# Performance work log

Measured on AMD Instinct MI355X. Metric: run time of the kernel, lower is better.

Reference implementation:

```python
import jax, jax.numpy as jnp
import numpy as np

B, C, T, H, W, L = 4, 256, 8, 16, 16, 8
NO = 8                # num_offsets
D = C // NO           # per-head feature dim for offset/weight MLPs
EPS = 1e-5


def setup_inputs() -> dict:
    key = jax.random.key(0)
    ks = jax.random.split(key, 6)
    return {
        "features": jax.random.normal(ks[0], (B, C, T, H, W, L), jnp.float32),
        "pos": jax.random.normal(ks[1], (B, C, T, H, W, L), jnp.float32),
        "Wp": jax.random.normal(ks[2], (C, 3 * C), jnp.float32) * 0.02,  # 1x1x1 conv: 3C -> C
        "bp": jnp.zeros((C,), jnp.float32),
        "Wo": jax.random.normal(ks[3], (D, 3), jnp.float32) * 0.02,      # offset_embed Linear(d,3)
        "bo": jnp.zeros((3,), jnp.float32),
        "Ww": jax.random.normal(ks[4], (D, 2), jnp.float32) * 0.02,      # weight_embed Linear(d,2)
        "bw": jnp.zeros((2,), jnp.float32),
    }


def _trilinear_sample(feat, coords):
    """feat: (N,C,D1,D2,D3); coords: (N,G,3) in [-1,1] (axis order D1,D2,D3).
    align_corners=False, zeros padding (matches F.grid_sample semantics)."""
    N, Cc, D1, D2, D3 = feat.shape
    sizes = jnp.asarray([D1, D2, D3], feat.dtype)
    pix = ((coords + 1.0) * sizes - 1.0) * 0.5       # unnormalize to pixel coords
    lo = jnp.floor(pix)
    frac = pix - lo                                   # (N,G,3)
    lo = lo.astype(jnp.int32)
    dims = jnp.asarray([D1, D2, D3], jnp.int32)
    feat_flat = feat.reshape(N, Cc, D1 * D2 * D3)
    out = jnp.zeros((N, Cc, coords.shape[1]), feat.dtype)
    for dz in (0, 1):
        for dy in (0, 1):
            for dx in (0, 1):
                off = jnp.asarray([dz, dy, dx], jnp.int32)
                idx = lo + off                        # (N,G,3)
                wz = jnp.where(dz, frac[..., 0], 1.0 - frac[..., 0])
                wy = jnp.where(dy, frac[..., 1], 1.0 - frac[..., 1])
                wx = jnp.where(dx, frac[..., 2], 1.0 - frac[..., 2])
                wgt = wz * wy * wx                    # (N,G)
                valid = jnp.all((idx >= 0) & (idx < dims), axis=-1)
                idc = jnp.clip(idx, 0, dims - 1)
                lin = (idc[..., 0] * D2 + idc[..., 1]) * D3 + idc[..., 2]  # (N,G)
                vals = jnp.take_along_axis(feat_flat, lin[:, None, :], axis=2)  # (N,C,G)
                out = out + vals * (wgt * valid)[:, None, :]
    return out


def reference(features, pos, Wp, bp, Wo, bo, Ww, bw):
    Bv, Cv, Tv, Hv, Wv, Lv = features.shape
    BT = Bv * Tv
    feat = features.transpose(0, 2, 1, 3, 4, 5).reshape(BT, Cv, Hv, Wv, Lv)
    posr = pos.transpose(0, 2, 1, 3, 4, 5).reshape(BT, Cv, Hv, Wv, Lv)
    # global context + projection (1x1x1 conv over 3C channels) + ReLU
    glob = feat.mean(axis=(2, 3, 4), keepdims=True)
    src = jnp.concatenate([feat, posr, jnp.broadcast_to(glob, feat.shape)], axis=1)  # (BT,3C,H,W,L)
    proj = jax.nn.relu(jnp.einsum('nixyz,oi->noxyz', src, Wp) + bp[None, :, None, None, None])
    osrc = proj.transpose(0, 2, 3, 4, 1).reshape(BT, Hv, Wv, Lv, NO, D)
    # per-voxel per-head offsets in (0,1) and scalar weights
    offset = jax.nn.sigmoid(osrc @ Wo + bo)                      # (BT,H,W,L,NO,3)
    wgt = jax.nn.softmax(osrc @ Ww + bw, axis=-1)[..., 1]        # (BT,H,W,L,NO)
    # base flow field in [-1,1], deform in logit space, re-sigmoid
    base = jnp.stack(jnp.meshgrid(jnp.linspace(-1.0, 1.0, Hv),
                                  jnp.linspace(-1.0, 1.0, Wv),
                                  jnp.linspace(-1.0, 1.0, Lv), indexing='ij'), axis=-1)
    base01 = jnp.clip((base + 1.0) * 0.5, EPS, 1.0 - EPS)
    logit = jnp.log(base01 / (1.0 - base01))                     # (H,W,L,3)
    sp = jax.nn.sigmoid(logit[None, :, :, :, None, :] + offset)  # (BT,H,W,L,NO,3)
    grid = (sp * 2.0 - 1.0).transpose(0, 4, 1, 2, 3, 5).reshape(BT, NO * Hv * Wv * Lv, 3)
    sampled = _trilinear_sample(feat, grid).reshape(BT, Cv, NO, Hv, Wv, Lv)
    out = feat + jnp.einsum('bcnhwl,bhwln->bchwl', sampled, wgt)
    return out.reshape(Bv, Tv, Cv, Hv, Wv, Lv).transpose(0, 2, 1, 3, 4, 5)
```

## Files before the change

### kernel.cpp

```cpp
#include <hip/hip_runtime.h>

#define BB 4
#define CC 256
#define TT 8
#define HH 16
#define WW 16
#define LL 8
#define NO 8
#define DD 32
#define BT 32
#define VV 2048
#define KIN 512
#define EPS_ 1e-5f

typedef short bf16x8 __attribute__((ext_vector_type(8)));
typedef float f32x4 __attribute__((ext_vector_type(4)));

static __device__ __forceinline__ float b2f(unsigned short u) {
    return __uint_as_float(((unsigned int)u) << 16);
}
static __device__ __forceinline__ float b2f_lo(unsigned int x) {
    return __uint_as_float(x << 16);
}
static __device__ __forceinline__ float b2f_hi(unsigned int x) {
    return __uint_as_float(x & 0xffff0000u);
}
static __device__ __forceinline__ unsigned short f2b(float f) {
    unsigned int x = __float_as_uint(f);
    unsigned int r = x + 0x7fffu + ((x >> 16) & 1u);
    return (unsigned short)(r >> 16);
}
static __device__ __forceinline__ unsigned int f2b_pk(float lo, float hi) {
    return (unsigned int)f2b(lo) | ((unsigned int)f2b(hi) << 16);
}
static __device__ __forceinline__ float sigm(float x) {
    return 1.0f / (1.0f + __expf(-x));
}
static __device__ __forceinline__ void glds16(const void* g, void* l) {
    __builtin_amdgcn_global_load_lds(
        (const __attribute__((address_space(1))) void*)g,
        (__attribute__((address_space(3))) void*)l, 16, 0, 0);
}

__global__ __launch_bounds__(256) void k0_prep(const float* __restrict__ Wp,
                                               unsigned short* __restrict__ Wa) {
    int i = blockIdx.x * 256 + threadIdx.x;
    int o = i >> 9, k = i & 511;
    Wa[i] = f2b(Wp[o * 768 + k]);
}

__global__ __launch_bounds__(256) void k1_transpose(const float* __restrict__ features,
                                                    const float* __restrict__ pos,
                                                    unsigned short* __restrict__ srcT,
                                                    float* __restrict__ gpart) {
    const int vt  = blockIdx.x;
    const int ch  = blockIdx.y & 1;
    const int arr = blockIdx.y >> 1;
    const int n   = blockIdx.z;
    const int v0 = vt * 64;
    const int b = n >> 3, t = n & 7;
    const int tid = threadIdx.x;
    const int w = tid >> 6;
    const int lane = tid & 63;
    const int cs  = lane >> 4;
    const int v16 = lane & 15;

    __shared__ float s1[64 * 132];

    const float* src = arr ? pos : features;
    const float* bp0 = src + ((size_t)(b * CC + ch * 128 + w * 32 + cs) * TT + t) * (size_t)VV
                           + v0 + v16 * 4;

    float4 fv[8];
    #pragma unroll
    for (int i = 0; i < 8; ++i)
        fv[i] = *(const float4*)(bp0 + (size_t)i * 4 * TT * VV);

    float part[8];
    #pragma unroll
    for (int i = 0; i < 8; ++i) {
        const int c_l = w * 32 + i * 4 + cs;
        float* dst = &s1[(v16 * 4) * 132 + c_l];
        dst[0 * 132] = fv[i].x;
        dst[1 * 132] = fv[i].y;
        dst[2 * 132] = fv[i].z;
        dst[3 * 132] = fv[i].w;
        part[i] = fv[i].x + fv[i].y + fv[i].z + fv[i].w;
    }

    if (arr == 0) {
        #pragma unroll
        for (int i = 0; i < 8; ++i) {
            #pragma unroll
            for (int m = 1; m < 16; m <<= 1)
                part[i] += __shfl_xor(part[i], m);
        }
        if (v16 == 0) {
            #pragma unroll
            for (int i = 0; i < 8; ++i)
                gpart[((size_t)n * 32 + vt) * CC + ch * 128 + w * 32 + i * 4 + cs] = part[i];
        }
    }
    __syncthreads();

    const int vo = tid >> 2, q = tid & 3;
    const float* row = &s1[vo * 132];
    unsigned short* ob = srcT + ((size_t)n * VV + v0 + vo) * KIN + arr * 256 + ch * 128;
    #pragma unroll
    for (int j = 0; j < 4; ++j) {
        const int c0 = j * 32 + q * 8;
        float4 f0 = *(const float4*)(row + c0);
        float4 f1 = *(const float4*)(row + c0 + 4);
        uint4 o;
        o.x = f2b_pk(f0.x, f0.y);
        o.y = f2b_pk(f0.z, f0.w);
        o.z = f2b_pk(f1.x, f1.y);
        o.w = f2b_pk(f1.z, f1.w);
        *(uint4*)(ob + c0) = o;
    }
}

__global__ __launch_bounds__(256) void k2_gterm(const float* __restrict__ gpart,
                                                const float* __restrict__ Wp,
                                                const float* __restrict__ bp,
                                                float* __restrict__ gterm) {
    const int n = blockIdx.x;
    const int o = threadIdx.x;
    __shared__ float gl[CC];
    float s = 0.0f;
    const float* gp = gpart + (size_t)n * 32 * CC + o;
    #pragma unroll 8
    for (int vt = 0; vt < 32; ++vt) s += gp[vt * CC];
    gl[o] = s * (1.0f / (float)VV);
    __syncthreads();
    const float4* wrow = (const float4*)(Wp + (size_t)o * 768 + 512);
    const float4* g4 = (const float4*)gl;
    float acc = bp[o];
    #pragma unroll 8
    for (int c = 0; c < 64; ++c) {
        float4 w = wrow[c], g = g4[c];
        acc += w.x * g.x + w.y * g.y + w.z * g.z + w.w * g.w;
    }
    gterm[n * CC + o] = acc;
}

__global__ __launch_bounds__(256) void k3_gemm(const unsigned short* __restrict__ Wa,
                                               const unsigned short* __restrict__ srcT,
                                               const float* __restrict__ gterm,
                                               unsigned short* __restrict__ projT) {
    const int n  = blockIdx.x;
    const int mb = blockIdx.y;
    const int nb = blockIdx.z;
    const int tid = threadIdx.x;
    const int m0 = mb * 128, v0 = nb * 128;

    __shared__ short As[128 * 32];
    __shared__ short Bs[128 * 32];

    const int w = tid >> 6;
    const int lane = tid & 63;
    const int wm = w >> 1, wn = w & 1;
    const int lr = lane & 15, lq = lane >> 4;

    f32x4 acc[4][4];
    #pragma unroll
    for (int i = 0; i < 4; ++i)
        #pragma unroll
        for (int j = 0; j < 4; ++j)
            acc[i][j] = (f32x4){0.f, 0.f, 0.f, 0.f};

    const int rsub = lane >> 2;
    const int ksub = (lane & 3) * 8;
    const unsigned short* agp = Wa   + (size_t)(m0 + w * 16 + rsub) * KIN + ksub;
    const unsigned short* bgp = srcT + ((size_t)n * VV + v0 + w * 16 + rsub) * KIN + ksub;
    short* alds0 = &As[(w * 16) * 32];
    short* alds1 = &As[(64 + w * 16) * 32];
    short* blds0 = &Bs[(w * 16) * 32];
    short* blds1 = &Bs[(64 + w * 16) * 32];

    for (int k0 = 0; k0 < KIN; k0 += 32) {
        __syncthreads();
        glds16(agp + k0,                   alds0);
        glds16(agp + k0 + (size_t)64 * KIN, alds1);
        glds16(bgp + k0,                   blds0);
        glds16(bgp + k0 + (size_t)64 * KIN, blds1);
        __syncthreads();

        bf16x8 af[4], bf[4];
        #pragma unroll
        for (int i = 0; i < 4; ++i)
            af[i] = *(const bf16x8*)&As[(wm * 64 + i * 16 + lr) * 32 + lq * 8];
        #pragma unroll
        for (int j = 0; j < 4; ++j)
            bf[j] = *(const bf16x8*)&Bs[(wn * 64 + j * 16 + lr) * 32 + lq * 8];
        #pragma unroll
        for (int i = 0; i < 4; ++i)
            #pragma unroll
            for (int j = 0; j < 4; ++j)
                acc[i][j] = __builtin_amdgcn_mfma_f32_16x16x32_bf16(af[i], bf[j], acc[i][j], 0, 0, 0);
    }

    #pragma unroll
    for (int i = 0; i < 4; ++i) {
        const int og = m0 + wm * 64 + i * 16 + lq * 4;
        float4 g = *(const float4*)(gterm + n * CC + og);
        #pragma unroll
        for (int j = 0; j < 4; ++j) {
            const int vg = v0 + wn * 64 + j * 16 + lr;
            float x0 = fmaxf(acc[i][j][0] + g.x, 0.0f);
            float x1 = fmaxf(acc[i][j][1] + g.y, 0.0f);
            float x2 = fmaxf(acc[i][j][2] + g.z, 0.0f);
            float x3 = fmaxf(acc[i][j][3] + g.w, 0.0f);
            ushort4 st;
            st.x = f2b(x0); st.y = f2b(x1); st.z = f2b(x2); st.w = f2b(x3);
            *(ushort4*)&projT[((size_t)n * VV + vg) * CC + og] = st;
        }
    }
}

__global__ __launch_bounds__(256) void k4_coef(const unsigned short* __restrict__ projT,
                                               const float* __restrict__ Wo,
                                               const float* __restrict__ bo,
                                               const float* __restrict__ Ww,
                                               const float* __restrict__ bw,
                                               int2* __restrict__ pairs) {
    __shared__ float sWo[96], sWw[64], sb[5];
    const int tid = threadIdx.x;
    if (tid < 96) sWo[tid] = Wo[tid];
    if (tid < 64) sWw[tid] = Ww[tid];
    if (tid < 3)  sb[tid] = bo[tid];
    if (tid < 2)  sb[3 + tid] = bw[tid];
    __syncthreads();

    const int g = blockIdx.x * 256 + tid;
    const int n = g >> 14;
    const int rem = g & 16383;
    const int v = rem >> 3;
    const int hd = rem & 7;

    const uint4* up = (const uint4*)(projT + ((size_t)n * VV + v) * CC + hd * DD);
    float osrc[32];
    #pragma unroll
    for (int q = 0; q < 4; ++q) {
        uint4 u = up[q];
        unsigned int ws4[4] = {u.x, u.y, u.z, u.w};
        #pragma unroll
        for (int e = 0; e < 4; ++e) {
            osrc[q * 8 + e * 2]     = b2f_lo(ws4[e]);
            osrc[q * 8 + e * 2 + 1] = b2f_hi(ws4[e]);
        }
    }

    float o0 = sb[0], o1 = sb[1], o2 = sb[2];
    float zw = sb[4] - sb[3];
    #pragma unroll
    for (int d = 0; d < DD; ++d) {
        float t = osrc[d];
        o0 += t * sWo[3 * d + 0];
        o1 += t * sWo[3 * d + 1];
        o2 += t * sWo[3 * d + 2];
        zw += t * (sWw[2 * d + 1] - sWw[2 * d]);
    }
    const float wgt = sigm(zw);

    const int h = v >> 7, w = (v >> 3) & 15, l = v & 7;
    float ph = fminf(fmaxf(h * (1.0f / 15.0f), EPS_), 1.0f - EPS_);
    float pw = fminf(fmaxf(w * (1.0f / 15.0f), EPS_), 1.0f - EPS_);
    float pl = fminf(fmaxf(l * (1.0f / 7.0f),  EPS_), 1.0f - EPS_);
    float lh = __logf(ph / (1.0f - ph));
    float lw = __logf(pw / (1.0f - pw));
    float ll = __logf(pl / (1.0f - pl));

    float sph = sigm(lh + sigm(o0));
    float spw = sigm(lw + sigm(o1));
    float spl = sigm(ll + sigm(o2));
    float pixh = sph * 16.0f - 0.5f;
    float pixw = spw * 16.0f - 0.5f;
    float pixl = spl * 8.0f  - 0.5f;

    float flh = floorf(pixh), flw = floorf(pixw), fll = floorf(pixl);
    float fh = pixh - flh, fw = pixw - flw, fl = pixl - fll;
    int ih = (int)flh, iw = (int)flw, il = (int)fll;

    int2* pp = pairs + (size_t)g * 8;
    #pragma unroll
    for (int dz = 0; dz < 2; ++dz)
        #pragma unroll
        for (int dy = 0; dy < 2; ++dy)
            #pragma unroll
            for (int dx = 0; dx < 2; ++dx) {
                int iz = ih + dz, iy = iw + dy, ix = il + dx;
                float wt = (dz ? fh : 1.0f - fh) * (dy ? fw : 1.0f - fw) * (dx ? fl : 1.0f - fl) * wgt;
                bool valid = ((unsigned)iz < 16u) && ((unsigned)iy < 16u) && ((unsigned)ix < 8u);
                int lin = valid ? (((iz * 16 + iy) * 8 + ix) << 10) : 0;
                float wv2 = valid ? wt : 0.0f;
                pp[dz * 4 + dy * 2 + dx] = make_int2(lin, __float_as_int(wv2));
            }
}

__global__ __launch_bounds__(256) void k5_gather(const unsigned short* __restrict__ srcT,
                                                 const int2* __restrict__ pairs,
                                                 unsigned short* __restrict__ res) {
    __shared__ int   sK[4 * 64];
    __shared__ float sW[4 * 64];
    const int tid = threadIdx.x;
    const int wid = tid >> 6;
    const int lane = tid & 63;
    const int gv = blockIdx.x * 4 + wid;
    const int n = gv >> 11;
    const int v = gv & 2047;

    int2 q = pairs[(size_t)gv * 64 + lane];
    int key = q.x;
    float w = __int_as_float(q.y);

    #pragma unroll
    for (int k = 2; k <= 64; k <<= 1) {
        #pragma unroll
        for (int j = k >> 1; j > 0; j >>= 1) {
            int pk = __shfl_xor(key, j);
            float pw = __shfl_xor(w, j);
            bool keepMin = (((lane & k) == 0) == ((lane & j) == 0));
            bool take = keepMin ? (pk < key) : (pk > key);
            if (take) { key = pk; w = pw; }
        }
    }
    #pragma unroll
    for (int d = 1; d < 64; d <<= 1) {
        float tw = __shfl_up(w, d);
        int   tk = __shfl_up(key, d);
        if (lane >= d && tk == key) w += tw;
    }
    int nk = __shfl_down(key, 1);
    bool tail = (lane == 63) || (nk != key);
    unsigned long long mask = __ballot(tail);
    int cnt = __popcll(mask);
    int cidx = __popcll(mask & ((1ull << lane) - 1ull));

    sK[wid * 64 + lane] = 0;
    sW[wid * 64 + lane] = 0.0f;
    __syncthreads();
    if (tail) { sK[wid * 64 + cidx] = key; sW[wid * 64 + cidx] = w; }
    __syncthreads();
    int ck = sK[wid * 64 + lane];
    float cw = sW[wid * 64 + lane];

    const char* slabB = (const char*)srcT + (size_t)n * VV * KIN * 2 + lane * 8;
    float a0 = 0.f, a1 = 0.f, a2 = 0.f, a3 = 0.f;
    const int iters = (cnt + 7) & ~7;
    #pragma unroll 1
    for (int e = 0; e < iters; e += 8) {
        uint2 f[8]; float wv[8];
        #pragma unroll
        for (int u = 0; u < 8; ++u) {
            int rk = __shfl(ck, e + u);
            wv[u] = __shfl(cw, e + u);
            f[u] = *(const uint2*)(slabB + (unsigned)rk);
        }
        #pragma unroll
        for (int u = 0; u < 8; ++u) {
            a0 = fmaf(wv[u], b2f_lo(f[u].x), a0);
            a1 = fmaf(wv[u], b2f_hi(f[u].x), a1);
            a2 = fmaf(wv[u], b2f_lo(f[u].y), a2);
            a3 = fmaf(wv[u], b2f_hi(f[u].y), a3);
        }
    }

    uint2 st;
    st.x = f2b_pk(a0, a1);
    st.y = f2b_pk(a2, a3);
    *(uint2*)&res[((size_t)n * VV + v) * CC + lane * 4] = st;
}

__global__ __launch_bounds__(256) void k6_final(const float* __restrict__ features,
                                                const unsigned short* __restrict__ res,
                                                float* __restrict__ out) {
    const int n = blockIdx.x;
    const int c0 = blockIdx.y * 64;
    const int v0 = blockIdx.z * 64;
    const int b = n >> 3, t = n & 7;
    const int tid = threadIdx.x;
    const int ty = tid >> 6, tx = tid & 63;

    __shared__ unsigned short t6[64 * 66];

    for (int vv = ty; vv < 64; vv += 4)
        t6[vv * 66 + tx] = res[((size_t)n * VV + v0 + vv) * CC + c0 + tx];
    __syncthreads();
    for (int cc = ty; cc < 64; cc += 4) {
        int c = c0 + cc;
        size_t oidx = (((size_t)b * CC + c) * TT + t) * VV + v0 + tx;
        out[oidx] = features[oidx] + b2f(t6[tx * 66 + cc]);
    }
}

extern "C" void kernel_launch(void* const* d_in, const int* in_sizes, int n_in,
                              void* d_out, int out_size, void* d_ws, size_t ws_size,
                              hipStream_t stream) {
    (void)in_sizes; (void)n_in; (void)out_size; (void)ws_size;
    const float* features = (const float*)d_in[0];
    const float* pos      = (const float*)d_in[1];
    const float* Wp       = (const float*)d_in[2];
    const float* bp       = (const float*)d_in[3];
    const float* Wo       = (const float*)d_in[4];
    const float* bo       = (const float*)d_in[5];
    const float* Ww       = (const float*)d_in[6];
    const float* bw       = (const float*)d_in[7];
    float* out = (float*)d_out;

    char* ws = (char*)d_ws;
    unsigned short* srcT  = (unsigned short*)ws;
    unsigned short* Wa    = (unsigned short*)(ws + 67108864);
    float*          gterm = (float*)(ws + 67403776);
    unsigned short* projT = (unsigned short*)(ws + 67436544);
    int2*           pairs = (int2*)(ws + 100990976);
    float*          gpart = (float*)(ws + 100990976);
    unsigned short* res   = projT;

    k0_prep<<<512, 256, 0, stream>>>(Wp, Wa);
    k1_transpose<<<dim3(32, 4, 32), 256, 0, stream>>>(features, pos, srcT, gpart);
    k2_gterm<<<32, 256, 0, stream>>>(gpart, Wp, bp, gterm);
    k3_gemm<<<dim3(32, 2, 16), 256, 0, stream>>>(Wa, srcT, gterm, projT);
    k4_coef<<<2048, 256, 0, stream>>>(projT, Wo, bo, Ww, bw, pairs);
    k5_gather<<<16384, 256, 0, stream>>>(srcT, pairs, res);
    k6_final<<<dim3(32, 4, 32), 256, 0, stream>>>(features, res, out);
}
```

Baseline: 330.5 us.

## Convert to bf16 before LDS transpose and use DPP/readlane in sort-gather kernel

The transpose kernel now packs fp32 values to bf16 pairs before staging them in shared memory. This halves LDS traffic and size, and it changes the lane mapping and the reduction pattern for the global-mean partial sums. The gather kernel's bitonic sort swaps generic shuffles for DPP and ds_swizzle cross-lane ops. Its gather loop uses readlane scalar broadcasts and packed f32x2 FMAs instead of per-lane shuffles and scalar fmaf. These touch several kernels and risk different rounding order in the partial sums and possible miscompiles of the DPP control codes.

```diff
diff --git a/kernel.cpp b/kernel.cpp
--- a/kernel.cpp
+++ b/kernel.cpp
@@ -15,6 +15,7 @@
 
 typedef short bf16x8 __attribute__((ext_vector_type(8)));
 typedef float f32x4 __attribute__((ext_vector_type(4)));
+typedef float f32x2 __attribute__((ext_vector_type(2)));
 
 static __device__ __forceinline__ float b2f(unsigned short u) {
     return __uint_as_float(((unsigned int)u) << 16);
@@ -40,6 +41,16 @@
     __builtin_amdgcn_global_load_lds(
         (const __attribute__((address_space(1))) void*)g,
         (__attribute__((address_space(3))) void*)l, 16, 0, 0);
+}
+static __device__ __forceinline__ int xsw(int x, int j) {
+    switch (j) {
+        case 1:  return __builtin_amdgcn_update_dpp(0, x, 0xB1, 0xF, 0xF, true);
+        case 2:  return __builtin_amdgcn_update_dpp(0, x, 0x4E, 0xF, 0xF, true);
+        case 8:  return __builtin_amdgcn_update_dpp(0, x, 0x128, 0xF, 0xF, true);
+        case 4:  return __builtin_amdgcn_ds_swizzle(x, 0x101F);
+        case 16: return __builtin_amdgcn_ds_swizzle(x, 0x401F);
+        default: return __shfl_xor(x, 32);
+    }
 }
 
 __global__ __launch_bounds__(256) void k0_prep(const float* __restrict__ Wp,
@@ -62,61 +73,68 @@
     const int tid = threadIdx.x;
     const int w = tid >> 6;
     const int lane = tid & 63;
-    const int cs  = lane >> 4;
-    const int v16 = lane & 15;
-
-    __shared__ float s1[64 * 132];
+    const int v16 = lane >> 2;
+    const int cs  = lane & 3;
+
+    __shared__ uint2 sg[64 * 33];
 
     const float* src = arr ? pos : features;
-    const float* bp0 = src + ((size_t)(b * CC + ch * 128 + w * 32 + cs) * TT + t) * (size_t)VV
-                           + v0 + v16 * 4;
-
-    float4 fv[8];
-    #pragma unroll
-    for (int i = 0; i < 8; ++i)
-        fv[i] = *(const float4*)(bp0 + (size_t)i * 4 * TT * VV);
-
-    float part[8];
-    #pragma unroll
-    for (int i = 0; i < 8; ++i) {
-        const int c_l = w * 32 + i * 4 + cs;
-        float* dst = &s1[(v16 * 4) * 132 + c_l];
-        dst[0 * 132] = fv[i].x;
-        dst[1 * 132] = fv[i].y;
-        dst[2 * 132] = fv[i].z;
-        dst[3 * 132] = fv[i].w;
-        part[i] = fv[i].x + fv[i].y + fv[i].z + fv[i].w;
+    const size_t cb = ((size_t)(b * CC + ch * 128 + w * 32) * TT + t) * (size_t)VV
+                      + v0 + v16 * 4;
+
+    float4 f[2][4];
+    #pragma unroll
+    for (int i = 0; i < 2; ++i)
+        #pragma unroll
+        for (int e = 0; e < 4; ++e)
+            f[i][e] = *(const float4*)(src + cb + (size_t)(i * 16 + cs * 4 + e) * (TT * VV));
+
+    #pragma unroll
+    for (int i = 0; i < 2; ++i) {
+        const int cq = w * 8 + i * 4 + cs;
+        #pragma unroll
+        for (int k = 0; k < 4; ++k) {
+            const int v = v16 * 4 + k;
+            uint2 u;
+            u.x = f2b_pk(((const float*)&f[i][0])[k], ((const float*)&f[i][1])[k]);
+            u.y = f2b_pk(((const float*)&f[i][2])[k], ((const float*)&f[i][3])[k]);
+            sg[v * 33 + cq] = u;
+        }
     }
 
     if (arr == 0) {
-        #pragma unroll
-        for (int i = 0; i < 8; ++i) {
+        float part[2][4];
+        #pragma unroll
+        for (int i = 0; i < 2; ++i)
             #pragma unroll
-            for (int m = 1; m < 16; m <<= 1)
-                part[i] += __shfl_xor(part[i], m);
-        }
-        if (v16 == 0) {
+            for (int e = 0; e < 4; ++e)
+                part[i][e] = f[i][e].x + f[i][e].y + f[i][e].z + f[i][e].w;
+        #pragma unroll
+        for (int i = 0; i < 2; ++i)
             #pragma unroll
-            for (int i = 0; i < 8; ++i)
-                gpart[((size_t)n * 32 + vt) * CC + ch * 128 + w * 32 + i * 4 + cs] = part[i];
-        }
-    }
-    __syncthreads();
-
-    const int vo = tid >> 2, q = tid & 3;
-    const float* row = &s1[vo * 132];
-    unsigned short* ob = srcT + ((size_t)n * VV + v0 + vo) * KIN + arr * 256 + ch * 128;
+            for (int e = 0; e < 4; ++e)
+                #pragma unroll
+                for (int m = 4; m < 64; m <<= 1)
+                    part[i][e] += __shfl_xor(part[i][e], m);
+        if (lane < 4) {
+            float* gp = gpart + ((size_t)n * 32 + vt) * CC + ch * 128 + w * 32 + cs * 4;
+            *(float4*)gp        = make_float4(part[0][0], part[0][1], part[0][2], part[0][3]);
+            *(float4*)(gp + 16) = make_float4(part[1][0], part[1][1], part[1][2], part[1][3]);
+        }
+    }
+    __syncthreads();
+
+    const int vh = tid >> 4;
+    const int q  = tid & 15;
+    unsigned short* ob = srcT + ((size_t)n * VV + v0) * KIN + arr * 256 + ch * 128 + q * 8;
     #pragma unroll
     for (int j = 0; j < 4; ++j) {
-        const int c0 = j * 32 + q * 8;
-        float4 f0 = *(const float4*)(row + c0);
-        float4 f1 = *(const float4*)(row + c0 + 4);
+        const int v = j * 16 + vh;
+        uint2 lo = sg[v * 33 + q * 2];
+        uint2 hi = sg[v * 33 + q * 2 + 1];
         uint4 o;
-        o.x = f2b_pk(f0.x, f0.y);
-        o.y = f2b_pk(f0.z, f0.w);
-        o.z = f2b_pk(f1.x, f1.y);
-        o.w = f2b_pk(f1.z, f1.w);
-        *(uint4*)(ob + c0) = o;
+        o.x = lo.x; o.y = lo.y; o.z = hi.x; o.w = hi.y;
+        *(uint4*)(ob + (size_t)v * KIN) = o;
     }
 }
 
@@ -180,9 +198,9 @@
 
     for (int k0 = 0; k0 < KIN; k0 += 32) {
         __syncthreads();
-        glds16(agp + k0,                   alds0);
+        glds16(agp + k0,                    alds0);
         glds16(agp + k0 + (size_t)64 * KIN, alds1);
-        glds16(bgp + k0,                   blds0);
+        glds16(bgp + k0,                    blds0);
         glds16(bgp + k0 + (size_t)64 * KIN, blds1);
         __syncthreads();
 
@@ -318,8 +336,8 @@
     for (int k = 2; k <= 64; k <<= 1) {
         #pragma unroll
         for (int j = k >> 1; j > 0; j >>= 1) {
-            int pk = __shfl_xor(key, j);
-            float pw = __shfl_xor(w, j);
+            int pk = xsw(key, j);
+            float pw = __int_as_float(xsw(__float_as_int(w), j));
             bool keepMin = (((lane & k) == 0) == ((lane & j) == 0));
             bool take = keepMin ? (pk < key) : (pk > key);
             if (take) { key = pk; w = pw; }
@@ -346,29 +364,28 @@
     float cw = sW[wid * 64 + lane];
 
     const char* slabB = (const char*)srcT + (size_t)n * VV * KIN * 2 + lane * 8;
-    float a0 = 0.f, a1 = 0.f, a2 = 0.f, a3 = 0.f;
+    f32x2 a01 = (f32x2){0.f, 0.f}, a23 = (f32x2){0.f, 0.f};
     const int iters = (cnt + 7) & ~7;
     #pragma unroll 1
     for (int e = 0; e < iters; e += 8) {
         uint2 f[8]; float wv[8];
         #pragma unroll
         for (int u = 0; u < 8; ++u) {
-            int rk = __shfl(ck, e + u);
-            wv[u] = __shfl(cw, e + u);
+            int rk = __builtin_amdgcn_readlane(ck, e + u);
+            wv[u] = __uint_as_float(
+                        __builtin_amdgcn_readlane(__float_as_uint(cw), e + u));
             f[u] = *(const uint2*)(slabB + (unsigned)rk);
         }
         #pragma unroll
         for (int u = 0; u < 8; ++u) {
-            a0 = fmaf(wv[u], b2f_lo(f[u].x), a0);
-            a1 = fmaf(wv[u], b2f_hi(f[u].x), a1);
-            a2 = fmaf(wv[u], b2f_lo(f[u].y), a2);
-            a3 = fmaf(wv[u], b2f_hi(f[u].y), a3);
+            a01 += wv[u] * (f32x2){b2f_lo(f[u].x), b2f_hi(f[u].x)};
+            a23 += wv[u] * (f32x2){b2f_lo(f[u].y), b2f_hi(f[u].y)};
         }
     }
 
     uint2 st;
-    st.x = f2b_pk(a0, a1);
-    st.y = f2b_pk(a2, a3);
+    st.x = f2b_pk(a01.x, a01.y);
+    st.y = f2b_pk(a23.x, a23.y);
     *(uint2*)&res[((size_t)n * VV + v) * CC + lane * 4] = st;
 }
 
```

After: 314.1 us. 1.05x faster.
